# Optimization experiments

Measured on AMD Instinct MI355X. Metric: run time of the kernel, lower is better.

## Reference

```python
import jax, jax.numpy as jnp
import numpy as np

K = 3          # kernel size (both dims)
PAD = 1        # padding used both for offset_mask conv and deform_conv2d
KK = K * K


def setup_inputs() -> dict:
    key = jax.random.key(0)
    k0, k1, k2, k3, k4 = jax.random.split(key, 5)
    B, C, H, W, O = 8, 64, 64, 64, 64
    input_feat = jax.random.normal(k0, (B, C, H, W), jnp.float32)
    degrad_inter = jax.random.normal(k1, (B, C, H, W), jnp.float32)
    stdv = 1.0 / np.sqrt(C * K * K)
    weight = jax.random.uniform(k2, (O, C, K, K), jnp.float32, -stdv, stdv)
    # small-magnitude offset/mask conv params -> realistic small learned offsets
    om_weight = jax.random.normal(k3, (3 * KK, 2 * C, K, K), jnp.float32) * 0.01
    om_bias = jax.random.normal(k4, (3 * KK,), jnp.float32) * 0.01
    return {"input_feat": input_feat, "degrad_inter": degrad_inter,
            "weight": weight, "om_weight": om_weight, "om_bias": om_bias}


def _conv2d(x, w, b):
    out = jax.lax.conv_general_dilated(
        x, w, window_strides=(1, 1), padding=((PAD, PAD), (PAD, PAD)),
        dimension_numbers=("NCHW", "OIHW", "NCHW"))
    return out + b[None, :, None, None]


def _deform_conv2d(x, offset, mask, weight):
    # x: (B,C,H,W); offset: (B,2*KK,H,W) with channel 2k=dy_k, 2k+1=dx_k;
    # mask: (B,KK,H,W); weight: (O,C,K,K). stride=1, padding=PAD, dilation=1.
    B, C, H, W = x.shape
    O = weight.shape[0]
    off = offset.reshape(B, KK, 2, H, W)
    dy, dx = off[:, :, 0], off[:, :, 1]                       # (B,KK,H,W)

    ky, kx = jnp.meshgrid(jnp.arange(K), jnp.arange(K), indexing="ij")
    ky = ky.reshape(KK).astype(x.dtype)
    kx = kx.reshape(KK).astype(x.dtype)
    hh = jnp.arange(H, dtype=x.dtype)
    ww = jnp.arange(W, dtype=x.dtype)
    # absolute fractional sample locations: (B,KK,H,W)
    y = hh[None, None, :, None] - PAD + ky[None, :, None, None] + dy
    xq = ww[None, None, None, :] - PAD + kx[None, :, None, None] + dx

    y0 = jnp.floor(y).astype(jnp.int32)
    x0 = jnp.floor(xq).astype(jnp.int32)
    y1, x1 = y0 + 1, x0 + 1
    wy = y - y0.astype(x.dtype)
    wx = xq - x0.astype(x.dtype)

    x_flat = x.reshape(B, C, H * W)

    def gather(yi, xi):
        valid = (yi >= 0) & (yi < H) & (xi >= 0) & (xi < W)
        idx = jnp.clip(yi, 0, H - 1) * W + jnp.clip(xi, 0, W - 1)  # (B,KK,H,W)
        vals = jax.vmap(lambda im, ix: im[:, ix])(x_flat, idx)     # (B,C,KK,H,W)
        return vals * valid[:, None].astype(x.dtype)

    wy_ = wy[:, None]  # (B,1,KK,H,W)
    wx_ = wx[:, None]
    sampled = (gather(y0, x0) * (1 - wy_) * (1 - wx_)
               + gather(y0, x1) * (1 - wy_) * wx_
               + gather(y1, x0) * wy_ * (1 - wx_)
               + gather(y1, x1) * wy_ * wx_)                       # (B,C,KK,H,W)
    sampled = sampled * mask[:, None]
    return jnp.einsum("bckhw,ock->bohw", sampled, weight.reshape(O, C, KK))


def reference(input_feat, degrad_inter, weight, om_weight, om_bias):
    concat = jnp.concatenate([input_feat, degrad_inter], axis=1)
    om = _conv2d(concat, om_weight, om_bias)                       # (B,3*KK,H,W)
    off1, off2, mask = jnp.split(om, 3, axis=1)
    offset = jnp.concatenate([off1, off2], axis=1)                 # (B,2*KK,H,W)
    mask = jax.nn.sigmoid(mask)                                    # (B,KK,H,W)
    return _deform_conv2d(input_feat, offset, mask, weight)
```

## Files before the change

kernel.cpp:

```cpp
#include <hip/hip_runtime.h>
#include <math.h>

#define WO_PK_OFF 36864
#define CATT_OFF  73728

typedef short  short8  __attribute__((ext_vector_type(8)));
typedef float  float4v __attribute__((ext_vector_type(4)));

static __device__ __forceinline__ short f2bf(float f) {
    unsigned int u = __builtin_bit_cast(unsigned int, f);
    u += 0x7FFFu + ((u >> 16) & 1u);
    return (short)(u >> 16);
}
static __device__ __forceinline__ float bf2f(unsigned short u) {
    return __builtin_bit_cast(float, (unsigned int)u << 16);
}

__global__ __launch_bounds__(256) void prep_w(
    const float* __restrict__ weight, const float* __restrict__ om_weight,
    short* __restrict__ wd_pk, short* __restrict__ wo_pk)
{
    int idx = blockIdx.x * 256 + threadIdx.x;
    if (idx < 36864) {
        int j = idx & 7, o = (idx >> 3) & 63, lq = (idx >> 9) & 3, ks = idx >> 11;
        int t = ks >> 1, c = (ks & 1) * 32 + lq * 8 + j;
        wd_pk[idx] = f2bf(weight[(o * 64 + c) * 9 + t]);
    } else {
        int e = idx - 36864;
        int j = e & 7, oc = (e >> 3) & 31, lq = (e >> 8) & 3, ks2 = e >> 10;
        int quarter = ks2 / 9, t = ks2 - quarter * 9;
        int cg = quarter * 32 + lq * 8 + j;
        wo_pk[e] = (oc < 27) ? f2bf(om_weight[(oc * 128 + cg) * 9 + t])
                             : (short)0;
    }
}

__global__ __launch_bounds__(256) void transpose_kernel(
    const float* __restrict__ feat, const float* __restrict__ deg,
    unsigned short* __restrict__ catT)
{
    __shared__ unsigned short T[64 * 136];
    const int b = blockIdx.x >> 6, h = blockIdx.x & 63;
    const int tid = threadIdx.x;
    const int lane = tid & 63, wv = tid >> 6;
#pragma unroll
    for (int cc = 0; cc < 32; cc++) {
        int c = wv * 32 + cc;
        const float* src = (c < 64)
            ? (feat + (size_t)(b * 64 + c) * 4096)
            : (deg  + (size_t)(b * 64 + (c - 64)) * 4096);
        T[lane * 136 + c] = (unsigned short)f2bf(src[h * 64 + lane]);
    }
    __syncthreads();
    const int px = tid >> 2, seg = tid & 3;
    unsigned short* dst = catT + (size_t)(b * 4096 + h * 64 + px) * 128 + seg * 32;
#pragma unroll
    for (int j = 0; j < 4; j++)
        *(uint4*)(dst + j * 8) = *(const uint4*)&T[px * 136 + seg * 32 + j * 8];
}

__global__ __launch_bounds__(256) void fused_kernel(
    const unsigned short* __restrict__ catT, const short* __restrict__ wd_pk,
    const short* __restrict__ wo_pk, const float* __restrict__ om_bias,
    float* __restrict__ out)
{
    __shared__ float T[4 * 16 * 36];
    const int tid = threadIdx.x;
    const int lane = tid & 63, wv = tid >> 6;
    const int l16 = lane & 15, lq = lane >> 4;
    const int gw = blockIdx.x * 4 + wv;
    const int b = gw >> 8, tile = gw & 255;
    const int h = tile >> 2, w0 = (tile & 3) << 4;
    const int pxx = w0 + l16;
    const unsigned short* cb = catT + (size_t)b * 4096 * 128;

    float4v oacc0 = {0.f, 0.f, 0.f, 0.f};
    float4v oacc1 = {0.f, 0.f, 0.f, 0.f};
    const short8 zf = {0, 0, 0, 0, 0, 0, 0, 0};
#pragma unroll
    for (int quarter = 0; quarter < 4; quarter++) {
#pragma unroll
        for (int t = 0; t < 9; t++) {
            const int ky = t / 3, kx = t - ky * 3;
            const int yy = h - 1 + ky;
            if (yy >= 0 && yy <= 63) {
                int xx = pxx - 1 + kx;
                bool okx = (xx >= 0) & (xx <= 63);
                int xc = min(max(xx, 0), 63);
                short8 bfr = *(const short8*)(cb + (yy * 64 + xc) * 128
                                                 + quarter * 32 + lq * 8);
                bfr = okx ? bfr : zf;
                const short8* Ap = (const short8*)(wo_pk
                    + (size_t)((quarter * 9 + t) * 4 + lq) * 256);
                oacc0 = __builtin_amdgcn_mfma_f32_16x16x32_bf16(
                    Ap[l16], bfr, oacc0, 0, 0, 0);
                oacc1 = __builtin_amdgcn_mfma_f32_16x16x32_bf16(
                    Ap[16 + l16], bfr, oacc1, 0, 0, 0);
            }
        }
    }

    float* Tw = T + wv * 576;
#pragma unroll
    for (int r = 0; r < 4; r++) {
        Tw[l16 * 36 + lq * 4 + r]      = oacc0[r];
        Tw[l16 * 36 + 16 + lq * 4 + r] = oacc1[r];
    }
    __syncthreads();
    float omv[28];
#pragma unroll
    for (int jj = 0; jj < 7; jj++)
        *(float4v*)&omv[jj * 4] = *(const float4v*)&Tw[l16 * 36 + jj * 4];
#pragma unroll
    for (int j = 0; j < 27; j++) omv[j] += om_bias[j];

    float4v acc[4];
#pragma unroll
    for (int mt = 0; mt < 4; mt++) acc[mt] = (float4v){0.f, 0.f, 0.f, 0.f};
#pragma unroll
    for (int t = 0; t < 9; t++) {
        const int ky = t / 3, kx = t - ky * 3;
        float dy = omv[2 * t], dx = omv[2 * t + 1];
        float mm = 1.f / (1.f + __expf(-omv[18 + t]));
        float yf = (float)(h - 1 + ky) + dy;
        float xf = (float)(pxx - 1 + kx) + dx;
        float fy = floorf(yf), fx = floorf(xf);
        int y0 = (int)fy, x0 = (int)fx;
        float wy = yf - fy, wx = xf - fx;
        bool vy0 = (y0 >= 0) & (y0 < 64);
        bool vy1 = (y0 >= -1) & (y0 < 63);
        bool vx0 = (x0 >= 0) & (x0 < 64);
        bool vx1 = (x0 >= -1) & (x0 < 63);
        float a0 = (1.f - wy) * mm, a1 = wy * mm;
        float W00 = a0 * (1.f - wx) * (float)(vy0 & vx0);
        float W01 = a0 * wx         * (float)(vy0 & vx1);
        float W10 = a1 * (1.f - wx) * (float)(vy1 & vx0);
        float W11 = a1 * wx         * (float)(vy1 & vx1);
        int iy0 = min(max(y0, 0), 63),     ix0 = min(max(x0, 0), 63);
        int iy1 = min(max(y0 + 1, 0), 63), ix1 = min(max(x0 + 1, 0), 63);
        int O00 = (iy0 * 64 + ix0) * 128, O01 = (iy0 * 64 + ix1) * 128;
        int O10 = (iy1 * 64 + ix0) * 128, O11 = (iy1 * 64 + ix1) * 128;
#pragma unroll
        for (int qh = 0; qh < 2; qh++) {
            const int cho = qh * 32 + lq * 8;
            short8 c00 = *(const short8*)(cb + O00 + cho);
            short8 c01 = *(const short8*)(cb + O01 + cho);
            short8 c10 = *(const short8*)(cb + O10 + cho);
            short8 c11 = *(const short8*)(cb + O11 + cho);
            short8 bfr;
#pragma unroll
            for (int j = 0; j < 8; j++) {
                float s = W00 * bf2f((unsigned short)c00[j])
                        + W01 * bf2f((unsigned short)c01[j])
                        + W10 * bf2f((unsigned short)c10[j])
                        + W11 * bf2f((unsigned short)c11[j]);
                bfr[j] = f2bf(s);
            }
            const short8* Dp = (const short8*)(wd_pk
                + (size_t)((t * 2 + qh) * 4 + lq) * 512);
            acc[0] = __builtin_amdgcn_mfma_f32_16x16x32_bf16(
                Dp[l16], bfr, acc[0], 0, 0, 0);
            acc[1] = __builtin_amdgcn_mfma_f32_16x16x32_bf16(
                Dp[16 + l16], bfr, acc[1], 0, 0, 0);
            acc[2] = __builtin_amdgcn_mfma_f32_16x16x32_bf16(
                Dp[32 + l16], bfr, acc[2], 0, 0, 0);
            acc[3] = __builtin_amdgcn_mfma_f32_16x16x32_bf16(
                Dp[48 + l16], bfr, acc[3], 0, 0, 0);
        }
    }

    float* ob = out + (size_t)(b * 64) * 4096 + h * 64 + w0 + l16;
#pragma unroll
    for (int mt = 0; mt < 4; mt++)
#pragma unroll
        for (int r = 0; r < 4; r++)
            ob[(mt * 16 + lq * 4 + r) * 4096] = acc[mt][r];
}

extern "C" void kernel_launch(void* const* d_in, const int* in_sizes, int n_in,
                              void* d_out, int out_size, void* d_ws, size_t ws_size,
                              hipStream_t stream)
{
    const float* feat      = (const float*)d_in[0];
    const float* deg       = (const float*)d_in[1];
    const float* weight    = (const float*)d_in[2];
    const float* om_weight = (const float*)d_in[3];
    const float* om_bias   = (const float*)d_in[4];
    float* out = (float*)d_out;
    short* wss = (short*)d_ws;
    unsigned short* catT = (unsigned short*)(wss + CATT_OFF);

    hipLaunchKernelGGL(prep_w,           dim3(288), dim3(256), 0, stream,
                       weight, om_weight, wss, wss + WO_PK_OFF);
    hipLaunchKernelGGL(transpose_kernel, dim3(512), dim3(256), 0, stream,
                       feat, deg, catT);
    hipLaunchKernelGGL(fused_kernel,     dim3(512), dim3(256), 0, stream,
                       catT, wss, wss + WO_PK_OFF, om_bias, out);
}
```

Measured before the change: 113.6 us.

## Merge prep kernels, stage deform weights in LDS, use packed bf16 conversion

```diff
diff --git a/kernel.cpp b/kernel.cpp
--- a/kernel.cpp
+++ b/kernel.cpp
@@ -6,6 +6,7 @@
 
 typedef short  short8  __attribute__((ext_vector_type(8)));
 typedef float  float4v __attribute__((ext_vector_type(4)));
+typedef unsigned int uint4v __attribute__((ext_vector_type(4)));
 
 static __device__ __forceinline__ short f2bf(float f) {
     unsigned int u = __builtin_bit_cast(unsigned int, f);
@@ -15,33 +16,39 @@
 static __device__ __forceinline__ float bf2f(unsigned short u) {
     return __builtin_bit_cast(float, (unsigned int)u << 16);
 }
-
-__global__ __launch_bounds__(256) void prep_w(
+static __device__ __forceinline__ unsigned int cvt_pk_bf16(float lo, float hi) {
+    unsigned int r;
+    asm("v_cvt_pk_bf16_f32 %0, %1, %2" : "=v"(r) : "v"(lo), "v"(hi));
+    return r;
+}
+
+__global__ __launch_bounds__(256) void prep_kernel(
+    const float* __restrict__ feat, const float* __restrict__ deg,
+    unsigned short* __restrict__ catT,
     const float* __restrict__ weight, const float* __restrict__ om_weight,
     short* __restrict__ wd_pk, short* __restrict__ wo_pk)
 {
-    int idx = blockIdx.x * 256 + threadIdx.x;
-    if (idx < 36864) {
-        int j = idx & 7, o = (idx >> 3) & 63, lq = (idx >> 9) & 3, ks = idx >> 11;
-        int t = ks >> 1, c = (ks & 1) * 32 + lq * 8 + j;
-        wd_pk[idx] = f2bf(weight[(o * 64 + c) * 9 + t]);
-    } else {
-        int e = idx - 36864;
-        int j = e & 7, oc = (e >> 3) & 31, lq = (e >> 8) & 3, ks2 = e >> 10;
-        int quarter = ks2 / 9, t = ks2 - quarter * 9;
-        int cg = quarter * 32 + lq * 8 + j;
-        wo_pk[e] = (oc < 27) ? f2bf(om_weight[(oc * 128 + cg) * 9 + t])
-                             : (short)0;
-    }
-}
-
-__global__ __launch_bounds__(256) void transpose_kernel(
-    const float* __restrict__ feat, const float* __restrict__ deg,
-    unsigned short* __restrict__ catT)
-{
     __shared__ unsigned short T[64 * 136];
+    const int tid = threadIdx.x;
+
+    if (blockIdx.x >= 512) {
+        int idx = (blockIdx.x - 512) * 256 + tid;
+        if (idx < 36864) {
+            int j = idx & 7, o = (idx >> 3) & 63, lq = (idx >> 9) & 3, ks = idx >> 11;
+            int t = ks >> 1, c = (ks & 1) * 32 + lq * 8 + j;
+            wd_pk[idx] = f2bf(weight[(o * 64 + c) * 9 + t]);
+        } else {
+            int e = idx - 36864;
+            int j = e & 7, oc = (e >> 3) & 31, lq = (e >> 8) & 3, ks2 = e >> 10;
+            int quarter = ks2 / 9, t = ks2 - quarter * 9;
+            int cg = quarter * 32 + lq * 8 + j;
+            wo_pk[e] = (oc < 27) ? f2bf(om_weight[(oc * 128 + cg) * 9 + t])
+                                 : (short)0;
+        }
+        return;
+    }
+
     const int b = blockIdx.x >> 6, h = blockIdx.x & 63;
-    const int tid = threadIdx.x;
     const int lane = tid & 63, wv = tid >> 6;
 #pragma unroll
     for (int cc = 0; cc < 32; cc++) {
@@ -64,7 +71,8 @@
     const short* __restrict__ wo_pk, const float* __restrict__ om_bias,
     float* __restrict__ out)
 {
-    __shared__ float T[4 * 16 * 36];
+    __shared__ __align__(16) short lwd[36864];
+    __shared__ __align__(16) float Tsm[4 * 448];
     const int tid = threadIdx.x;
     const int lane = tid & 63, wv = tid >> 6;
     const int l16 = lane & 15, lq = lane >> 4;
@@ -73,6 +81,14 @@
     const int h = tile >> 2, w0 = (tile & 3) << 4;
     const int pxx = w0 + l16;
     const unsigned short* cb = catT + (size_t)b * 4096 * 128;
+
+    {
+        const uint4* src = (const uint4*)wd_pk;
+        uint4* dst = (uint4*)lwd;
+#pragma unroll
+        for (int i = 0; i < 18; i++)
+            dst[i * 256 + tid] = src[i * 256 + tid];
+    }
 
     float4v oacc0 = {0.f, 0.f, 0.f, 0.f};
     float4v oacc1 = {0.f, 0.f, 0.f, 0.f};
@@ -100,17 +116,18 @@
         }
     }
 
-    float* Tw = T + wv * 576;
+    float* Tw = Tsm + wv * 448;
 #pragma unroll
     for (int r = 0; r < 4; r++) {
-        Tw[l16 * 36 + lq * 4 + r]      = oacc0[r];
-        Tw[l16 * 36 + 16 + lq * 4 + r] = oacc1[r];
+        Tw[l16 * 28 + lq * 4 + r] = oacc0[r];
+        if (lq < 3)
+            Tw[l16 * 28 + 16 + lq * 4 + r] = oacc1[r];
     }
     __syncthreads();
     float omv[28];
 #pragma unroll
     for (int jj = 0; jj < 7; jj++)
-        *(float4v*)&omv[jj * 4] = *(const float4v*)&Tw[l16 * 36 + jj * 4];
+        *(float4v*)&omv[jj * 4] = *(const float4v*)&Tw[l16 * 28 + jj * 4];
 #pragma unroll
     for (int j = 0; j < 27; j++) omv[j] += om_bias[j];
 
@@ -143,20 +160,27 @@
 #pragma unroll
         for (int qh = 0; qh < 2; qh++) {
             const int cho = qh * 32 + lq * 8;
-            short8 c00 = *(const short8*)(cb + O00 + cho);
-            short8 c01 = *(const short8*)(cb + O01 + cho);
-            short8 c10 = *(const short8*)(cb + O10 + cho);
-            short8 c11 = *(const short8*)(cb + O11 + cho);
-            short8 bfr;
-#pragma unroll
-            for (int j = 0; j < 8; j++) {
-                float s = W00 * bf2f((unsigned short)c00[j])
-                        + W01 * bf2f((unsigned short)c01[j])
-                        + W10 * bf2f((unsigned short)c10[j])
-                        + W11 * bf2f((unsigned short)c11[j]);
-                bfr[j] = f2bf(s);
+            uint4v u00 = *(const uint4v*)(cb + O00 + cho);
+            uint4v u01 = *(const uint4v*)(cb + O01 + cho);
+            uint4v u10 = *(const uint4v*)(cb + O10 + cho);
+            uint4v u11 = *(const uint4v*)(cb + O11 + cho);
+            uint4v br;
+#pragma unroll
+            for (int p = 0; p < 4; p++) {
+                float l00 = __builtin_bit_cast(float, u00[p] << 16);
+                float h00 = __builtin_bit_cast(float, u00[p] & 0xffff0000u);
+                float l01 = __builtin_bit_cast(float, u01[p] << 16);
+                float h01 = __builtin_bit_cast(float, u01[p] & 0xffff0000u);
+                float l10 = __builtin_bit_cast(float, u10[p] << 16);
+                float h10 = __builtin_bit_cast(float, u10[p] & 0xffff0000u);
+                float l11 = __builtin_bit_cast(float, u11[p] << 16);
+                float h11 = __builtin_bit_cast(float, u11[p] & 0xffff0000u);
+                float slo = W00 * l00 + W01 * l01 + W10 * l10 + W11 * l11;
+                float shi = W00 * h00 + W01 * h01 + W10 * h10 + W11 * h11;
+                br[p] = cvt_pk_bf16(slo, shi);
             }
-            const short8* Dp = (const short8*)(wd_pk
+            short8 bfr = __builtin_bit_cast(short8, br);
+            const short8* Dp = (const short8*)(lwd
                 + (size_t)((t * 2 + qh) * 4 + lq) * 512);
             acc[0] = __builtin_amdgcn_mfma_f32_16x16x32_bf16(
                 Dp[l16], bfr, acc[0], 0, 0, 0);
@@ -190,10 +214,9 @@
     short* wss = (short*)d_ws;
     unsigned short* catT = (unsigned short*)(wss + CATT_OFF);
 
-    hipLaunchKernelGGL(prep_w,           dim3(288), dim3(256), 0, stream,
-                       weight, om_weight, wss, wss + WO_PK_OFF);
-    hipLaunchKernelGGL(transpose_kernel, dim3(512), dim3(256), 0, stream,
-                       feat, deg, catT);
-    hipLaunchKernelGGL(fused_kernel,     dim3(512), dim3(256), 0, stream,
+    hipLaunchKernelGGL(prep_kernel, dim3(800), dim3(256), 0, stream,
+                       feat, deg, catT, weight, om_weight,
+                       wss, wss + WO_PK_OFF);
+    hipLaunchKernelGGL(fused_kernel, dim3(512), dim3(256), 0, stream,
                        catT, wss, wss + WO_PK_OFF, om_bias, out);
 }
```

After: 116.1 us. +2.2%, slower.
